# Kernel optimization log

Measured on AMD Instinct MI355X. Metric: run time of the kernel, lower is better.

The kernel has to match this reference:

```python
import jax, jax.numpy as jnp
import numpy as np

FEATURE_DIM = 1024
N_CONCEPTS = 32768
BATCH = 1024
TEMPERATURE = 0.1
EPS = 1e-12  # matches torch F.normalize eps


def l2_normalize(x, axis=-1):
    n = jnp.linalg.norm(x, axis=axis, keepdims=True)
    return x / jnp.maximum(n, EPS)


def setup_inputs() -> dict:
    key = jax.random.key(0)
    k1, k2, k3, k4 = jax.random.split(key, 4)
    features = jax.random.normal(k1, (BATCH, FEATURE_DIM), dtype=jnp.float32)
    # Linear projection params (original inits to identity/zeros; random exercises the math)
    W = jnp.eye(FEATURE_DIM, dtype=jnp.float32) + 0.02 * jax.random.normal(k2, (FEATURE_DIM, FEATURE_DIM), dtype=jnp.float32)
    b = 0.01 * jax.random.normal(k3, (FEATURE_DIM,), dtype=jnp.float32)
    prototypes = l2_normalize(jax.random.normal(k4, (N_CONCEPTS, FEATURE_DIM), dtype=jnp.float32))
    return {"features": features, "W": W, "b": b, "prototypes": prototypes}


def reference(features, W, b, prototypes):
    # projection: features @ W.T + b   (torch nn.Linear convention)
    projected = jnp.einsum('bd,ed->be', features, W) + b          # [B, D]
    projected = l2_normalize(projected)                           # [B, D]
    # cosine similarity against all prototypes
    similarities = jnp.einsum('bd,kd->bk', projected, prototypes) # [B, K]
    activations = jax.nn.softmax(similarities / TEMPERATURE, axis=-1)
    best_idx = jnp.argmax(similarities, axis=-1)                  # [B] int
    return activations, best_idx
```

## Files before the change

kernel.cpp:

```cpp
#include <hip/hip_runtime.h>
#include <hip/hip_bf16.h>


typedef __attribute__((ext_vector_type(8))) short short8;
typedef __attribute__((ext_vector_type(4))) float floatx4;

__device__ __forceinline__ unsigned short f2bf(float f) {
  unsigned int u = __float_as_uint(f);
  u += 0x7fffu + ((u >> 16) & 1u);
  return (unsigned short)(u >> 16);
}
__device__ __forceinline__ float bf2f(unsigned short h) {
  return __uint_as_float(((unsigned int)h) << 16);
}

__global__ __launch_bounds__(256) void cvt_f32_bf16(
    const float* __restrict__ src, unsigned short* __restrict__ dst, int n8) {
  int i = blockIdx.x * blockDim.x + threadIdx.x;
  if (i >= n8) return;
  const float4* s4 = (const float4*)src;
  float4 a = s4[2 * i];
  float4 b = s4[2 * i + 1];
  short8 o;
  o[0] = (short)f2bf(a.x); o[1] = (short)f2bf(a.y);
  o[2] = (short)f2bf(a.z); o[3] = (short)f2bf(a.w);
  o[4] = (short)f2bf(b.x); o[5] = (short)f2bf(b.y);
  o[6] = (short)f2bf(b.z); o[7] = (short)f2bf(b.w);
  ((short8*)dst)[i] = o;
}

__global__ __launch_bounds__(256) void cvt_split3(
    const float* __restrict__ src, unsigned short* __restrict__ H,
    unsigned short* __restrict__ Md, unsigned short* __restrict__ L, int n4) {
  int i = blockIdx.x * blockDim.x + threadIdx.x;
  if (i >= n4) return;
  float4 x = ((const float4*)src)[i];
  ushort4 h, m, l;
  float v, r;
  v = x.x; h.x = f2bf(v); r = v - bf2f(h.x); m.x = f2bf(r); l.x = f2bf(r - bf2f(m.x));
  v = x.y; h.y = f2bf(v); r = v - bf2f(h.y); m.y = f2bf(r); l.y = f2bf(r - bf2f(m.y));
  v = x.z; h.z = f2bf(v); r = v - bf2f(h.z); m.z = f2bf(r); l.z = f2bf(r - bf2f(m.z));
  v = x.w; h.w = f2bf(v); r = v - bf2f(h.w); m.w = f2bf(r); l.w = f2bf(r - bf2f(m.w));
  ((ushort4*)H)[i] = h; ((ushort4*)Md)[i] = m; ((ushort4*)L)[i] = l;
}

__global__ __launch_bounds__(256) void gemm_nt_bf16(
    const unsigned short* __restrict__ A, const unsigned short* __restrict__ B,
    float* __restrict__ C, int M, int N, int K) {
  __shared__ unsigned short As[128 * 32];
  __shared__ unsigned short Bs[128 * 32];
  const int tid  = threadIdx.x;
  const int wave = tid >> 6;
  const int lane = tid & 63;
  const long tm = (long)blockIdx.y * 128;
  const long tn = (long)blockIdx.x * 128;
  const int wm = (wave & 1) * 64;
  const int wn = (wave >> 1) * 64;

  floatx4 acc[4][4];
#pragma unroll
  for (int i = 0; i < 4; i++)
#pragma unroll
    for (int j = 0; j < 4; j++) acc[i][j] = (floatx4){0.f, 0.f, 0.f, 0.f};

  const int rstage = tid >> 2;
  const int cstage = (tid & 3) * 8;
  const unsigned short* Abase = A + (tm + rstage) * (long)K + cstage;
  const unsigned short* Bbase = B + (tn + rstage) * (long)K + cstage;

  for (int k0 = 0; k0 < K; k0 += 32) {
    __builtin_amdgcn_global_load_lds(
        (const __attribute__((address_space(1))) void*)(Abase + k0),
        (__attribute__((address_space(3))) void*)(As + wave * 512), 16, 0, 0);
    __builtin_amdgcn_global_load_lds(
        (const __attribute__((address_space(1))) void*)(Abase + 64 * (long)K + k0),
        (__attribute__((address_space(3))) void*)(As + 2048 + wave * 512), 16, 0, 0);
    __builtin_amdgcn_global_load_lds(
        (const __attribute__((address_space(1))) void*)(Bbase + k0),
        (__attribute__((address_space(3))) void*)(Bs + wave * 512), 16, 0, 0);
    __builtin_amdgcn_global_load_lds(
        (const __attribute__((address_space(1))) void*)(Bbase + 64 * (long)K + k0),
        (__attribute__((address_space(3))) void*)(Bs + 2048 + wave * 512), 16, 0, 0);
    __syncthreads();

    short8 af[4], bfv[4];
    const int fr = lane & 15;
    const int koff = (lane >> 4) * 8;
#pragma unroll
    for (int mf = 0; mf < 4; mf++)
      af[mf] = *(const short8*)(As + (wm + mf * 16 + fr) * 32 + koff);
#pragma unroll
    for (int nf = 0; nf < 4; nf++)
      bfv[nf] = *(const short8*)(Bs + (wn + nf * 16 + fr) * 32 + koff);
#pragma unroll
    for (int mf = 0; mf < 4; mf++)
#pragma unroll
      for (int nf = 0; nf < 4; nf++)
        acc[mf][nf] = __builtin_amdgcn_mfma_f32_16x16x32_bf16(
            af[mf], bfv[nf], acc[mf][nf], 0, 0, 0);
    __syncthreads();
  }

  const long crow = tm + wm + ((lane >> 4) * 4);
  const long ccol = tn + wn + (lane & 15);
#pragma unroll
  for (int mf = 0; mf < 4; mf++)
#pragma unroll
    for (int nf = 0; nf < 4; nf++)
#pragma unroll
      for (int r = 0; r < 4; r++)
        C[(crow + mf * 16 + r) * (long)N + ccol + nf * 16] = acc[mf][nf][r];
}

__global__ __launch_bounds__(256) void gemm_split6_nt(
    const unsigned short* __restrict__ Ah, const unsigned short* __restrict__ Am,
    const unsigned short* __restrict__ Al, const unsigned short* __restrict__ Bh,
    const unsigned short* __restrict__ Bm, const unsigned short* __restrict__ Bl,
    float* __restrict__ Cpart, int M, int N, int K) {
  __shared__ unsigned short sA[3][64 * 32];
  __shared__ unsigned short sB[3][64 * 32];
  const int tid  = threadIdx.x;
  const int wave = tid >> 6;
  const int lane = tid & 63;
  const long tm = (long)blockIdx.y * 64;
  const long tn = (long)blockIdx.x * 64;
  const int wm = (wave & 1) * 32;
  const int wn = (wave >> 1) * 32;
  const int ksize = K / gridDim.z;
  const int kbase = blockIdx.z * ksize;
  float* C = Cpart + (size_t)blockIdx.z * M * N;

  floatx4 accH[2][2], accL[2][2];
#pragma unroll
  for (int i = 0; i < 2; i++)
#pragma unroll
    for (int j = 0; j < 2; j++) {
      accH[i][j] = (floatx4){0.f, 0.f, 0.f, 0.f};
      accL[i][j] = (floatx4){0.f, 0.f, 0.f, 0.f};
    }

  const int rstage = tid >> 2;
  const int cstage = (tid & 3) * 8;
  const long aoff = (tm + rstage) * (long)K + cstage;
  const long boff = (tn + rstage) * (long)K + cstage;
  const unsigned short* Asrc[3] = {Ah + aoff, Am + aoff, Al + aoff};
  const unsigned short* Bsrc[3] = {Bh + boff, Bm + boff, Bl + boff};

  for (int k0 = kbase; k0 < kbase + ksize; k0 += 32) {
#pragma unroll
    for (int p = 0; p < 3; p++) {
      __builtin_amdgcn_global_load_lds(
          (const __attribute__((address_space(1))) void*)(Asrc[p] + k0),
          (__attribute__((address_space(3))) void*)(sA[p] + wave * 512), 16, 0, 0);
      __builtin_amdgcn_global_load_lds(
          (const __attribute__((address_space(1))) void*)(Bsrc[p] + k0),
          (__attribute__((address_space(3))) void*)(sB[p] + wave * 512), 16, 0, 0);
    }
    __syncthreads();

    const int fr = lane & 15;
    const int koff = (lane >> 4) * 8;
    short8 a_[3][2], b_[3][2];
#pragma unroll
    for (int p = 0; p < 3; p++)
#pragma unroll
      for (int mf = 0; mf < 2; mf++) {
        a_[p][mf] = *(const short8*)(sA[p] + (wm + mf * 16 + fr) * 32 + koff);
        b_[p][mf] = *(const short8*)(sB[p] + (wn + mf * 16 + fr) * 32 + koff);
      }
#pragma unroll
    for (int mf = 0; mf < 2; mf++)
#pragma unroll
      for (int nf = 0; nf < 2; nf++) {
        accH[mf][nf] = __builtin_amdgcn_mfma_f32_16x16x32_bf16(
            a_[0][mf], b_[0][nf], accH[mf][nf], 0, 0, 0);
        accL[mf][nf] = __builtin_amdgcn_mfma_f32_16x16x32_bf16(
            a_[0][mf], b_[1][nf], accL[mf][nf], 0, 0, 0);
        accL[mf][nf] = __builtin_amdgcn_mfma_f32_16x16x32_bf16(
            a_[1][mf], b_[0][nf], accL[mf][nf], 0, 0, 0);
        accL[mf][nf] = __builtin_amdgcn_mfma_f32_16x16x32_bf16(
            a_[0][mf], b_[2][nf], accL[mf][nf], 0, 0, 0);
        accL[mf][nf] = __builtin_amdgcn_mfma_f32_16x16x32_bf16(
            a_[2][mf], b_[0][nf], accL[mf][nf], 0, 0, 0);
        accL[mf][nf] = __builtin_amdgcn_mfma_f32_16x16x32_bf16(
            a_[1][mf], b_[1][nf], accL[mf][nf], 0, 0, 0);
      }
    __syncthreads();
  }

  const long crow = tm + wm + ((lane >> 4) * 4);
  const long ccol = tn + wn + (lane & 15);
#pragma unroll
  for (int mf = 0; mf < 2; mf++)
#pragma unroll
    for (int nf = 0; nf < 2; nf++)
#pragma unroll
      for (int r = 0; r < 4; r++)
        C[(crow + mf * 16 + r) * (long)N + ccol + nf * 16] =
            accH[mf][nf][r] + accL[mf][nf][r];
}

__global__ __launch_bounds__(256) void norm_bias_rows(
    const float* __restrict__ P0, const float* __restrict__ P1, int nparts,
    const float* __restrict__ bias, unsigned short* __restrict__ Pn,
    float* __restrict__ Pn32) {
  const int b = blockIdx.x, tid = threadIdx.x;
  float4 v = ((const float4*)(P0 + (long)b * 1024))[tid];
  if (nparts == 2) {
    float4 v1 = ((const float4*)(P1 + (long)b * 1024))[tid];
    v.x += v1.x; v.y += v1.y; v.z += v1.z; v.w += v1.w;
  }
  float4 bb = ((const float4*)bias)[tid];
  v.x += bb.x; v.y += bb.y; v.z += bb.z; v.w += bb.w;
  float ss = v.x * v.x + v.y * v.y + v.z * v.z + v.w * v.w;
#pragma unroll
  for (int off = 32; off > 0; off >>= 1) ss += __shfl_down(ss, off);
  __shared__ float wred[4];
  if ((tid & 63) == 0) wred[tid >> 6] = ss;
  __syncthreads();
  float tot = wred[0] + wred[1] + wred[2] + wred[3];
  float inv = 1.0f / fmaxf(sqrtf(tot), 1e-12f);
  float4 p = make_float4(v.x * inv, v.y * inv, v.z * inv, v.w * inv);
  ((float4*)Pn32)[b * 256 + tid] = p;
  ushort4 o;
  o.x = f2bf(p.x); o.y = f2bf(p.y); o.z = f2bf(p.z); o.w = f2bf(p.w);
  ((ushort4*)Pn)[b * 256 + tid] = o;
}

__global__ __launch_bounds__(256) void softmax_argmax_refine(
    float* __restrict__ S, const float* __restrict__ Pn32,
    const float* __restrict__ protos, float* __restrict__ idx_out) {
  const int b = blockIdx.x, tid = threadIdx.x;
  const int wave = tid >> 6, lane = tid & 63;
  float4* row4 = (float4*)(S + (long)b * 32768);

  float m = -3.4e38f, l = 0.f;
#pragma unroll 4
  for (int it = 0; it < 32; it++) {
    float4 v = row4[tid + 256 * it];
    float zx = v.x * 10.f, zy = v.y * 10.f, zz = v.z * 10.f, zw = v.w * 10.f;
    float m4 = fmaxf(fmaxf(zx, zy), fmaxf(zz, zw));
    float nm = fmaxf(m, m4);
    l = l * __expf(m - nm) + __expf(zx - nm) + __expf(zy - nm) +
        __expf(zz - nm) + __expf(zw - nm);
    m = nm;
  }
#pragma unroll
  for (int off = 1; off < 64; off <<= 1) {
    float mo = __shfl_xor(m, off);
    float lo = __shfl_xor(l, off);
    float nm = fmaxf(m, mo);
    l = l * __expf(m - nm) + lo * __expf(mo - nm);
    m = nm;
  }
  __shared__ float sm_[4], sl_[4];
  __shared__ int cand[64];
  __shared__ int ncand;
  if (lane == 0) { sm_[wave] = m; sl_[wave] = l; }
  if (tid == 0) ncand = 0;
  __syncthreads();
  float Mz = fmaxf(fmaxf(sm_[0], sm_[1]), fmaxf(sm_[2], sm_[3]));
  float L = sl_[0] * __expf(sm_[0] - Mz) + sl_[1] * __expf(sm_[1] - Mz) +
            sl_[2] * __expf(sm_[2] - Mz) + sl_[3] * __expf(sm_[3] - Mz);
  float invL = 1.0f / L;
  float thr = Mz * 0.1f - 0.012f;

#pragma unroll 4
  for (int it = 0; it < 32; it++) {
    int i4 = tid + 256 * it;
    float4 v = row4[i4];
    if (fmaxf(fmaxf(v.x, v.y), fmaxf(v.z, v.w)) >= thr) {
      if (v.x >= thr) { int p = atomicAdd(&ncand, 1); if (p < 64) cand[p] = i4 * 4; }
      if (v.y >= thr) { int p = atomicAdd(&ncand, 1); if (p < 64) cand[p] = i4 * 4 + 1; }
      if (v.z >= thr) { int p = atomicAdd(&ncand, 1); if (p < 64) cand[p] = i4 * 4 + 2; }
      if (v.w >= thr) { int p = atomicAdd(&ncand, 1); if (p < 64) cand[p] = i4 * 4 + 3; }
    }
    float4 e;
    e.x = __expf(v.x * 10.f - Mz) * invL;
    e.y = __expf(v.y * 10.f - Mz) * invL;
    e.z = __expf(v.z * 10.f - Mz) * invL;
    e.w = __expf(v.w * 10.f - Mz) * invL;
    row4[i4] = e;
  }
  __syncthreads();
  int n = ncand < 64 ? ncand : 64;

  float4 pv = ((const float4*)(Pn32 + (long)b * 1024))[tid];
  __shared__ double dred[4];
  double best = -1e300;
  int besti = 0x7fffffff;
  for (int c = 0; c < n; c++) {
    int k = cand[c];
    float4 kv = ((const float4*)(protos + (long)k * 1024))[tid];
    double d = (double)pv.x * kv.x + (double)pv.y * kv.y +
               (double)pv.z * kv.z + (double)pv.w * kv.w;
#pragma unroll
    for (int off = 32; off > 0; off >>= 1) d += __shfl_down(d, off);
    if (lane == 0) dred[wave] = d;
    __syncthreads();
    if (tid == 0) {
      double tot = dred[0] + dred[1] + dred[2] + dred[3];
      if (tot > best || (tot == best && k < besti)) { best = tot; besti = k; }
    }
    __syncthreads();
  }
  if (tid == 0) idx_out[b] = (float)besti;
}

extern "C" void kernel_launch(void* const* d_in, const int* in_sizes, int n_in,
                              void* d_out, int out_size, void* d_ws, size_t ws_size,
                              hipStream_t stream) {
  const float* features = (const float*)d_in[0];
  const float* W        = (const float*)d_in[1];
  const float* bias     = (const float*)d_in[2];
  const float* protos   = (const float*)d_in[3];

  const size_t MB = 1024 * 1024;
  char* ws = (char*)d_ws;
  unsigned short* protoB = (unsigned short*)ws;
  unsigned short* Fh = (unsigned short*)(ws + 64 * MB);
  unsigned short* Fm = (unsigned short*)(ws + 66 * MB);
  unsigned short* Fl = (unsigned short*)(ws + 68 * MB);
  unsigned short* Wh = (unsigned short*)(ws + 70 * MB);
  unsigned short* Wm = (unsigned short*)(ws + 72 * MB);
  unsigned short* Wl = (unsigned short*)(ws + 74 * MB);
  float*          P0 = (float*)(ws + 76 * MB);
  float*          P1 = (float*)(ws + 80 * MB);
  unsigned short* Pn   = (unsigned short*)(ws + 64 * MB);
  float*          Pn32 = (float*)(ws + 66 * MB);

  const int ksplit = (ws_size >= 84 * MB) ? 2 : 1;

  float* S = (float*)d_out;
  float* idx_out = S + (size_t)1024 * 32768;

  cvt_f32_bf16<<<16384, 256, 0, stream>>>(protos, protoB, 32768 * 1024 / 8);
  cvt_split3<<<1024, 256, 0, stream>>>(features, Fh, Fm, Fl, 1024 * 1024 / 4);
  cvt_split3<<<1024, 256, 0, stream>>>(W, Wh, Wm, Wl, 1024 * 1024 / 4);
  gemm_split6_nt<<<dim3(16, 16, ksplit), 256, 0, stream>>>(
      Fh, Fm, Fl, Wh, Wm, Wl, P0, 1024, 1024, 1024);
  norm_bias_rows<<<1024, 256, 0, stream>>>(P0, P1, ksplit, bias, Pn, Pn32);
  gemm_nt_bf16<<<dim3(256, 8), 256, 0, stream>>>(Pn, protoB, S, 1024, 32768, 1024);
  softmax_argmax_refine<<<1024, 256, 0, stream>>>(S, Pn32, protos, idx_out);
}
```

Measured before the change: 438.6 us.

## Replace main bf16 GEMM with 256x256 double-buffered, swizzled-LDS pipelined kernel

Swaps the 128x128 single-buffered similarity GEMM for a 256x256 tile kernel with 8 waves and a K-step of 64. LDS is double-buffered and XOR-swizzled, and global-to-LDS loads are interleaved with MFMA clusters using explicit barriers, waitcnts and setprio. Blocks are remapped so that groups share B tiles for better cache reuse. The aim is to hide memory latency and raise MFMA utilisation, but the hardcoded K=1024 and dimensions reduce generality, and the manual schedule is fragile.

```diff
diff --git a/kernel.cpp b/kernel.cpp
--- a/kernel.cpp
+++ b/kernel.cpp
@@ -44,72 +44,158 @@
   ((ushort4*)H)[i] = h; ((ushort4*)Md)[i] = m; ((ushort4*)L)[i] = l;
 }
 
-__global__ __launch_bounds__(256) void gemm_nt_bf16(
+
+#define BARRIER() asm volatile("s_barrier" ::: "memory")
+#define WAITLGKM()                                        \
+  do {                                                    \
+    asm volatile("s_waitcnt lgkmcnt(0)" ::: "memory");    \
+    __builtin_amdgcn_sched_barrier(0);                    \
+  } while (0)
+#define WAITVM4() asm volatile("s_waitcnt vmcnt(4)" ::: "memory")
+
+#define STAGE(OP, SLOT, H, KT)                                                 \
+  do {                                                                         \
+    const unsigned short* _s0 = (OP ? pB0 : pA0) + (H)*131072 + (KT)*64;       \
+    const unsigned short* _s1 = (OP ? pB1 : pA1) + (H)*131072 + (KT)*64;       \
+    __builtin_amdgcn_global_load_lds(                                          \
+        (const __attribute__((address_space(1))) void*)_s0,                    \
+        (__attribute__((address_space(3))) void*)(&lds[SLOT][OP][(H)*8192 + w * 512]), \
+        16, 0, 0);                                                             \
+    __builtin_amdgcn_global_load_lds(                                          \
+        (const __attribute__((address_space(1))) void*)_s1,                    \
+        (__attribute__((address_space(3))) void*)(&lds[SLOT][OP][(H)*8192 + 4096 + w * 512]), \
+        16, 0, 0);                                                             \
+  } while (0)
+
+#define READ4(dst, base, off, rowadd)                                          \
+  _Pragma("unroll") for (int q = 0; q < 4; q++)                                \
+      dst[q] = *(const short8*)((base) + (off) + ((rowadd) + q) * 2048);
+
+#define MFMA16(AB, BB, MBASE)                                                  \
+  do {                                                                         \
+    __builtin_amdgcn_sched_barrier(0);                                         \
+    __builtin_amdgcn_s_setprio(1);                                             \
+    _Pragma("unroll") for (int mf = 0; mf < 4; mf++)                           \
+        _Pragma("unroll") for (int nf = 0; nf < 4; nf++)                       \
+            acc[(MBASE) + mf][nf] = __builtin_amdgcn_mfma_f32_16x16x32_bf16(   \
+                AB[mf], BB[nf], acc[(MBASE) + mf][nf], 0, 0, 0);               \
+    __builtin_amdgcn_s_setprio(0);                                             \
+    __builtin_amdgcn_sched_barrier(0);                                         \
+  } while (0)
+
+__global__ __launch_bounds__(512, 2) void gemm_nt_bf16_256(
     const unsigned short* __restrict__ A, const unsigned short* __restrict__ B,
     float* __restrict__ C, int M, int N, int K) {
-  __shared__ unsigned short As[128 * 32];
-  __shared__ unsigned short Bs[128 * 32];
-  const int tid  = threadIdx.x;
-  const int wave = tid >> 6;
-  const int lane = tid & 63;
-  const long tm = (long)blockIdx.y * 128;
-  const long tn = (long)blockIdx.x * 128;
-  const int wm = (wave & 1) * 64;
-  const int wn = (wave >> 1) * 64;
-
-  floatx4 acc[4][4];
-#pragma unroll
-  for (int i = 0; i < 4; i++)
+  __shared__ unsigned short lds[2][2][16384];
+  const int tid = threadIdx.x;
+  const int w = tid >> 6, lane = tid & 63;
+  const int wr = w >> 2, wc = w & 3;
+  const int fr = lane & 15, koff8 = lane >> 4;
+
+  const int bid = blockIdx.x;
+  const int c8 = bid & 7, u = bid >> 3;
+  const long tn = (long)(c8 * 16 + (u >> 2)) * 256;
+  const long tm = (long)(u & 3) * 256;
+
+  const int idx0 = w * 64 + lane;
+  const int idx1 = 512 + idx0;
+  const int rh0 = idx0 >> 3, sc0 = (idx0 & 7) ^ (rh0 & 7);
+  const int rh1 = idx1 >> 3, sc1 = (idx1 & 7) ^ (rh1 & 7);
+  const unsigned short* pA0 = A + (tm + rh0) * 1024 + sc0 * 8;
+  const unsigned short* pA1 = A + (tm + rh1) * 1024 + sc1 * 8;
+  const unsigned short* pB0 = B + (tn + rh0) * 1024 + sc0 * 8;
+  const unsigned short* pB1 = B + (tn + rh1) * 1024 + sc1 * 8;
+
+  const int rA = wr * 128 + fr;
+  const int rB = wc * 64 + fr;
+  const int offA0 = rA * 128 + ((koff8 ^ (rA & 7)) << 4);
+  const int offA1 = rA * 128 + (((koff8 ^ 4) ^ (rA & 7)) << 4);
+  const int offB0 = rB * 128 + ((koff8 ^ (rB & 7)) << 4);
+  const int offB1 = rB * 128 + (((koff8 ^ 4) ^ (rB & 7)) << 4);
+
+  const char* ldsc = (const char*)&lds[0][0][0];
+#define LDSA(s) (ldsc + (s)*65536)
+#define LDSB(s) (ldsc + (s)*65536 + 32768)
+
+  floatx4 acc[8][4];
+#pragma unroll
+  for (int i = 0; i < 8; i++)
 #pragma unroll
     for (int j = 0; j < 4; j++) acc[i][j] = (floatx4){0.f, 0.f, 0.f, 0.f};
 
-  const int rstage = tid >> 2;
-  const int cstage = (tid & 3) * 8;
-  const unsigned short* Abase = A + (tm + rstage) * (long)K + cstage;
-  const unsigned short* Bbase = B + (tn + rstage) * (long)K + cstage;
-
-  for (int k0 = 0; k0 < K; k0 += 32) {
-    __builtin_amdgcn_global_load_lds(
-        (const __attribute__((address_space(1))) void*)(Abase + k0),
-        (__attribute__((address_space(3))) void*)(As + wave * 512), 16, 0, 0);
-    __builtin_amdgcn_global_load_lds(
-        (const __attribute__((address_space(1))) void*)(Abase + 64 * (long)K + k0),
-        (__attribute__((address_space(3))) void*)(As + 2048 + wave * 512), 16, 0, 0);
-    __builtin_amdgcn_global_load_lds(
-        (const __attribute__((address_space(1))) void*)(Bbase + k0),
-        (__attribute__((address_space(3))) void*)(Bs + wave * 512), 16, 0, 0);
-    __builtin_amdgcn_global_load_lds(
-        (const __attribute__((address_space(1))) void*)(Bbase + 64 * (long)K + k0),
-        (__attribute__((address_space(3))) void*)(Bs + 2048 + wave * 512), 16, 0, 0);
-    __syncthreads();
-
-    short8 af[4], bfv[4];
-    const int fr = lane & 15;
-    const int koff = (lane >> 4) * 8;
-#pragma unroll
-    for (int mf = 0; mf < 4; mf++)
-      af[mf] = *(const short8*)(As + (wm + mf * 16 + fr) * 32 + koff);
-#pragma unroll
-    for (int nf = 0; nf < 4; nf++)
-      bfv[nf] = *(const short8*)(Bs + (wn + nf * 16 + fr) * 32 + koff);
-#pragma unroll
-    for (int mf = 0; mf < 4; mf++)
-#pragma unroll
-      for (int nf = 0; nf < 4; nf++)
-        acc[mf][nf] = __builtin_amdgcn_mfma_f32_16x16x32_bf16(
-            af[mf], bfv[nf], acc[mf][nf], 0, 0, 0);
-    __syncthreads();
-  }
-
-  const long crow = tm + wm + ((lane >> 4) * 4);
-  const long ccol = tn + wn + (lane & 15);
-#pragma unroll
-  for (int mf = 0; mf < 4; mf++)
+  short8 a0[4], a1[4], a2[4], b0[4], b1[4];
+
+  STAGE(0, 0, 0, 0); STAGE(0, 0, 1, 0); STAGE(1, 0, 0, 0); STAGE(1, 0, 1, 0);
+  STAGE(0, 1, 0, 1); STAGE(0, 1, 1, 1);
+  WAITVM4();
+  BARRIER();
+
+#pragma unroll 1
+  for (int i = 0; i < 8; i++) {
+    const int t1 = 2 * i + 1;
+    const int t2 = (2 * i + 2) & 15;
+    const int t3 = (2 * i + 3) & 15;
+
+    READ4(a0, LDSA(0), offA0, 0);
+    READ4(a1, LDSA(0), offA0, 4);
+    READ4(b0, LDSB(0), offB0, 0);
+    STAGE(1, 1, 0, t1);
+    BARRIER(); WAITLGKM();
+    MFMA16(a0, b0, 0);
+    BARRIER();
+    READ4(a0, LDSA(0), offA1, 0);
+    READ4(a2, LDSA(0), offA1, 4);
+    READ4(b1, LDSB(0), offB1, 0);
+    STAGE(1, 1, 1, t1);
+    BARRIER(); WAITLGKM();
+    MFMA16(a1, b0, 4);
+    BARRIER();
+    STAGE(0, 0, 0, t2);
+    BARRIER();
+    MFMA16(a0, b1, 0);
+    BARRIER();
+    STAGE(0, 0, 1, t2);
+    WAITVM4();
+    BARRIER();
+    MFMA16(a2, b1, 4);
+    BARRIER();
+
+    READ4(a0, LDSA(1), offA0, 0);
+    READ4(a1, LDSA(1), offA0, 4);
+    READ4(b0, LDSB(1), offB0, 0);
+    STAGE(1, 0, 0, t2);
+    BARRIER(); WAITLGKM();
+    MFMA16(a0, b0, 0);
+    BARRIER();
+    READ4(a0, LDSA(1), offA1, 0);
+    READ4(a2, LDSA(1), offA1, 4);
+    READ4(b1, LDSB(1), offB1, 0);
+    STAGE(1, 0, 1, t2);
+    BARRIER(); WAITLGKM();
+    MFMA16(a1, b0, 4);
+    BARRIER();
+    STAGE(0, 1, 0, t3);
+    BARRIER();
+    MFMA16(a0, b1, 0);
+    BARRIER();
+    STAGE(0, 1, 1, t3);
+    WAITVM4();
+    BARRIER();
+    MFMA16(a2, b1, 4);
+    BARRIER();
+  }
+
+  const long crow = tm + wr * 128 + ((lane >> 4) * 4);
+  const long ccol = tn + wc * 64 + fr;
+#pragma unroll
+  for (int mf = 0; mf < 8; mf++)
 #pragma unroll
     for (int nf = 0; nf < 4; nf++)
 #pragma unroll
       for (int r = 0; r < 4; r++)
         C[(crow + mf * 16 + r) * (long)N + ccol + nf * 16] = acc[mf][nf][r];
+#undef LDSA
+#undef LDSB
 }
 
 __global__ __launch_bounds__(256) void gemm_split6_nt(
@@ -340,6 +426,6 @@
   gemm_split6_nt<<<dim3(16, 16, ksplit), 256, 0, stream>>>(
       Fh, Fm, Fl, Wh, Wm, Wl, P0, 1024, 1024, 1024);
   norm_bias_rows<<<1024, 256, 0, stream>>>(P0, P1, ksplit, bias, Pn, Pn32);
-  gemm_nt_bf16<<<dim3(256, 8), 256, 0, stream>>>(Pn, protoB, S, 1024, 32768, 1024);
+  gemm_nt_bf16_256<<<512, 512, 0, stream>>>(Pn, protoB, S, 1024, 32768, 1024);
   softmax_argmax_refine<<<1024, 256, 0, stream>>>(S, Pn32, protos, idx_out);
 }
```

New measurement: 410.0 us. 6.5% less time.
